# Optimization experiments

Measured on AMD Instinct MI355X. Metric: run time of the kernel, lower is better.

## Reference

```python
import jax, jax.numpy as jnp
import numpy as np

N_HEADS = 16
WINDOW_SIZE = 128


def setup_inputs() -> dict:
    key = jax.random.key(0)
    ks = jax.random.split(key, 5)
    B, T, D = 2, 2048, 1024
    x = jax.random.normal(ks[0], (B, T, D), dtype=jnp.float32)
    w_qkv = jax.random.normal(ks[1], (3 * D, D), dtype=jnp.float32) * (D ** -0.5)
    b_qkv = jax.random.normal(ks[2], (3 * D,), dtype=jnp.float32) * 0.01
    w_out = jax.random.normal(ks[3], (D, D), dtype=jnp.float32) * (D ** -0.5)
    b_out = jax.random.normal(ks[4], (D,), dtype=jnp.float32) * 0.01
    return {"x": x, "w_qkv": w_qkv, "b_qkv": b_qkv, "w_out": w_out, "b_out": b_out}


def reference(x, w_qkv, b_qkv, w_out, b_out):
    B, T, D = x.shape
    H = N_HEADS
    hd = D // H
    scale = hd ** -0.5

    # qkv projection: (B,T,3D) -> (3,B,H,T,hd)
    qkv = (x @ w_qkv.T + b_qkv).reshape(B, T, 3, H, hd)
    qkv = jnp.transpose(qkv, (2, 0, 3, 1, 4))
    q, k, v = qkv[0], qkv[1], qkv[2]

    pos = jnp.arange(T)
    # mask[i, j]: |j - i| <= w/2 and j >= i  (faithful to original, which
    # due to its index orientation allows query i to attend to keys j >= i)
    mask = (jnp.abs(pos[None, :] - pos[:, None]) <= WINDOW_SIZE // 2) & (
        pos[None, :] >= pos[:, None]
    )

    attn = jnp.einsum("bhqd,bhkd->bhqk", q, k) * scale  # (B,H,T,T)
    attn = jnp.where(mask[None, None], attn, -jnp.inf)
    attn = jax.nn.softmax(attn, axis=-1)
    attn = jnp.nan_to_num(attn, nan=0.0)

    out = jnp.einsum("bhqk,bhkd->bhqd", attn, v)  # (B,H,T,hd)
    out = jnp.transpose(out, (0, 2, 1, 3)).reshape(B, T, D)
    return out @ w_out.T + b_out
```

## Files before the change

kernel.cpp:

```cpp
#include <hip/hip_runtime.h>
#include <hip/hip_bf16.h>
#include <stdint.h>


typedef short bf16x8 __attribute__((ext_vector_type(8)));
typedef float f32x4 __attribute__((ext_vector_type(4)));

typedef const __attribute__((address_space(1))) void* gptr_t;
typedef __attribute__((address_space(3))) void* lptr_t;

__device__ __forceinline__ float bf2f(short u) {
    union { float f; uint32_t i; } x;
    x.i = ((uint32_t)(uint16_t)u) << 16;
    return x.f;
}
__device__ __forceinline__ short f2bf(float f) {
    __hip_bfloat16 h = __float2bfloat16(f);
    return *reinterpret_cast<short*>(&h);
}

__global__ __launch_bounds__(256)
void convert_all(const float* __restrict__ x, const float* __restrict__ wq,
                 const float* __restrict__ bq, const float* __restrict__ wo,
                 const float* __restrict__ bo,
                 short* __restrict__ xb, short* __restrict__ wqb, short* __restrict__ bqb,
                 short* __restrict__ wob, short* __restrict__ bob) {
    int i = blockIdx.x * 256 + threadIdx.x;
    const float* src; short* dst; int o;
    if      (i <  524288) { src = x;  dst = xb;  o = i; }
    else if (i <  917504) { src = wq; dst = wqb; o = i - 524288; }
    else if (i <  917888) { src = bq; dst = bqb; o = i - 917504; }
    else if (i < 1048960) { src = wo; dst = wob; o = i - 917888; }
    else if (i < 1049088) { src = bo; dst = bob; o = i - 1048960; }
    else return;
    const int e = o * 8;
    float4 a = *(const float4*)(src + e);
    float4 b = *(const float4*)(src + e + 4);
    short t[8];
    t[0] = f2bf(a.x); t[1] = f2bf(a.y); t[2] = f2bf(a.z); t[3] = f2bf(a.w);
    t[4] = f2bf(b.x); t[5] = f2bf(b.y); t[6] = f2bf(b.z); t[7] = f2bf(b.w);
    *(uint4*)(dst + e) = *(const uint4*)t;
}

__global__ __launch_bounds__(256)
void gemm_bt_128(const short* __restrict__ A, const short* __restrict__ Bt,
                 const short* __restrict__ bias, short* __restrict__ C,
                 int M, int N, int K) {
    __shared__ short As[128 * 32];
    __shared__ short Bs[128 * 32];

    const int tid  = threadIdx.x;
    const int lane = tid & 63;
    const int w    = tid >> 6;
    const int qd   = lane >> 4;
    const int l16  = lane & 15;
    const int wm   = w >> 1;
    const int wn   = w & 1;
    const int mBase = blockIdx.y * 128;
    const int nBase = blockIdx.x * 128;

    f32x4 acc[4][4] = {};

    const int nK = K >> 5;
    for (int kt = 0; kt < nK; ++kt) {
        const int kb = kt << 5;
#pragma unroll
        for (int i = 0; i < 2; ++i) {
            const int e   = i * 2048 + tid * 8;
            const int row = e >> 5;
            const int col = e & 31;
            const short* ga = A  + (size_t)(mBase + row) * K + kb + col;
            const short* gb = Bt + (size_t)(nBase + row) * K + kb + col;
            lptr_t la = (lptr_t)(As + i * 2048 + w * 512);
            lptr_t lb = (lptr_t)(Bs + i * 2048 + w * 512);
            __builtin_amdgcn_global_load_lds((gptr_t)ga, la, 16, 0, 0);
            __builtin_amdgcn_global_load_lds((gptr_t)gb, lb, 16, 0, 0);
        }
        __syncthreads();

        bf16x8 af[4], bfr[4];
#pragma unroll
        for (int mi = 0; mi < 4; ++mi)
            af[mi] = *(const bf16x8*)(As + (wm * 64 + mi * 16 + l16) * 32 + qd * 8);
#pragma unroll
        for (int ni = 0; ni < 4; ++ni)
            bfr[ni] = *(const bf16x8*)(Bs + (wn * 64 + ni * 16 + l16) * 32 + qd * 8);
#pragma unroll
        for (int mi = 0; mi < 4; ++mi)
#pragma unroll
            for (int ni = 0; ni < 4; ++ni)
                acc[mi][ni] = __builtin_amdgcn_mfma_f32_16x16x32_bf16(
                    bfr[ni], af[mi], acc[mi][ni], 0, 0, 0);
        __syncthreads();
    }

#pragma unroll
    for (int ni = 0; ni < 4; ++ni) {
        const int n0 = nBase + wn * 64 + ni * 16 + qd * 4;
        float bv[4];
#pragma unroll
        for (int r = 0; r < 4; ++r) bv[r] = bf2f(bias[n0 + r]);
#pragma unroll
        for (int mi = 0; mi < 4; ++mi) {
            const int m = mBase + wm * 64 + mi * 16 + l16;
            short t[4];
#pragma unroll
            for (int r = 0; r < 4; ++r) t[r] = f2bf(acc[mi][ni][r] + bv[r]);
            *(uint2*)&C[(size_t)m * N + n0] = *(const uint2*)t;
        }
    }
}

__global__ __launch_bounds__(256)
void gemm_bt_64(const short* __restrict__ A, const short* __restrict__ Bt,
                const short* __restrict__ bias, float* __restrict__ C,
                int M, int N, int K) {
    __shared__ short As[64 * 32];
    __shared__ short Bs[128 * 32];

    const int tid  = threadIdx.x;
    const int lane = tid & 63;
    const int w    = tid >> 6;
    const int qd   = lane >> 4;
    const int l16  = lane & 15;
    const int wm   = w >> 1;
    const int wn   = w & 1;
    const int mBase = blockIdx.y * 64;
    const int nBase = blockIdx.x * 128;

    f32x4 acc[2][4] = {};

    const int nK = K >> 5;
    for (int kt = 0; kt < nK; ++kt) {
        const int kb = kt << 5;
        {
            const int e   = tid * 8;
            const int row = e >> 5;
            const int col = e & 31;
            const short* ga = A + (size_t)(mBase + row) * K + kb + col;
            lptr_t la = (lptr_t)(As + w * 512);
            __builtin_amdgcn_global_load_lds((gptr_t)ga, la, 16, 0, 0);
        }
#pragma unroll
        for (int i = 0; i < 2; ++i) {
            const int e   = i * 2048 + tid * 8;
            const int row = e >> 5;
            const int col = e & 31;
            const short* gb = Bt + (size_t)(nBase + row) * K + kb + col;
            lptr_t lb = (lptr_t)(Bs + i * 2048 + w * 512);
            __builtin_amdgcn_global_load_lds((gptr_t)gb, lb, 16, 0, 0);
        }
        __syncthreads();

        bf16x8 af[2], bfr[4];
#pragma unroll
        for (int mi = 0; mi < 2; ++mi)
            af[mi] = *(const bf16x8*)(As + (wm * 32 + mi * 16 + l16) * 32 + qd * 8);
#pragma unroll
        for (int ni = 0; ni < 4; ++ni)
            bfr[ni] = *(const bf16x8*)(Bs + (wn * 64 + ni * 16 + l16) * 32 + qd * 8);
#pragma unroll
        for (int mi = 0; mi < 2; ++mi)
#pragma unroll
            for (int ni = 0; ni < 4; ++ni)
                acc[mi][ni] = __builtin_amdgcn_mfma_f32_16x16x32_bf16(
                    bfr[ni], af[mi], acc[mi][ni], 0, 0, 0);
        __syncthreads();
    }

#pragma unroll
    for (int ni = 0; ni < 4; ++ni) {
        const int n0 = nBase + wn * 64 + ni * 16 + qd * 4;
        float bv[4];
#pragma unroll
        for (int r = 0; r < 4; ++r) bv[r] = bf2f(bias[n0 + r]);
#pragma unroll
        for (int mi = 0; mi < 2; ++mi) {
            const int m = mBase + wm * 32 + mi * 16 + l16;
            f32x4 o;
#pragma unroll
            for (int r = 0; r < 4; ++r) o[r] = acc[mi][ni][r] + bv[r];
            *(f32x4*)&C[(size_t)m * N + n0] = o;
        }
    }
}

__global__ __launch_bounds__(256)
void attn_mfma(const short* __restrict__ qkv, short* __restrict__ attn_out, int B, int T) {
    __shared__ short k_s[128 * 72];
    __shared__ short v_s[144 * 66];
    __shared__ short p_s[64 * 104];

    const int tid  = threadIdx.x;
    const int lane = tid & 63;
    const int w    = tid >> 6;
    const int qd   = lane >> 4;
    const int l16  = lane & 15;
    const int qs   = blockIdx.x * 64;
    const int h    = blockIdx.y;
    const int b    = blockIdx.z;
    const size_t rs   = 3072;
    const size_t base = (size_t)b * T * rs;
    const int qoff = h * 64, koff = 1024 + h * 64, voff = 2048 + h * 64;

#pragma unroll
    for (int i = 0; i < 5; ++i) {
        const int c   = tid + i * 256;
        const int row = c >> 3;
        if (row >= 144) break;
        const int ch = (c & 7) * 8;
        int gr = qs + row; if (gr > T - 1) gr = T - 1;
        uint4 uv = *(const uint4*)(qkv + base + (size_t)gr * rs + voff + ch);
        if (row < 128) {
            uint4 uk = *(const uint4*)(qkv + base + (size_t)gr * rs + koff + ch);
            *(uint4*)&k_s[row * 72 + ch] = uk;
        }
        const uint32_t* vp = (const uint32_t*)&uv;
        uint32_t* vd = (uint32_t*)&v_s[row * 66 + ch];
        vd[0] = vp[0]; vd[1] = vp[1]; vd[2] = vp[2]; vd[3] = vp[3];
    }
    __syncthreads();

    bf16x8 aq0, aq1;
    {
        const short* g = qkv + base + (size_t)(qs + 16 * w + l16) * rs + qoff + qd * 8;
        aq0 = *(const bf16x8*)(g);
        aq1 = *(const bf16x8*)(g + 32);
    }

    f32x4 sacc[5] = {};
#pragma unroll
    for (int u = 0; u < 5; ++u) {
        const int krow = 16 * (w + u) + l16;
        bf16x8 bk0 = *(const bf16x8*)&k_s[krow * 72 + qd * 8];
        bf16x8 bk1 = *(const bf16x8*)&k_s[krow * 72 + 32 + qd * 8];
        sacc[u] = __builtin_amdgcn_mfma_f32_16x16x32_bf16(aq0, bk0, sacc[u], 0, 0, 0);
        sacc[u] = __builtin_amdgcn_mfma_f32_16x16x32_bf16(aq1, bk1, sacc[u], 0, 0, 0);
    }

    const float scale = 0.125f;
    float pw[5][4];
    float inv[4];
#pragma unroll
    for (int r = 0; r < 4; ++r) {
        const int m = 4 * qd + r;
        float mx = -3.4e38f;
#pragma unroll
        for (int u = 0; u < 5; ++u) {
            const int rel = 16 * u + l16 - m;
            const int j   = qs + 16 * (w + u) + l16;
            const bool ok = (rel >= 0) & (rel <= 64) & (j < T);
            const float v = ok ? sacc[u][r] * scale : -3.4e38f;
            pw[u][r] = v;
            mx = fmaxf(mx, v);
        }
#pragma unroll
        for (int msk = 1; msk <= 8; msk <<= 1) mx = fmaxf(mx, __shfl_xor(mx, msk));
        float sum = 0.f;
#pragma unroll
        for (int u = 0; u < 5; ++u) {
            float e = (pw[u][r] <= -3.0e38f) ? 0.f : __expf(pw[u][r] - mx);
            pw[u][r] = e;
            sum += e;
        }
#pragma unroll
        for (int msk = 1; msk <= 8; msk <<= 1) sum += __shfl_xor(sum, msk);
        inv[r] = 1.0f / sum;
    }

#pragma unroll
    for (int u = 0; u < 5; ++u)
#pragma unroll
        for (int r = 0; r < 4; ++r)
            p_s[(16 * w + 4 * qd + r) * 104 + 16 * u + l16] = f2bf(pw[u][r] * inv[r]);
#pragma unroll
    for (int r = 0; r < 4; ++r)
        p_s[(16 * w + 4 * qd + r) * 104 + 80 + l16] = 0;

    f32x4 oacc[4] = {};
#pragma unroll
    for (int ks = 0; ks < 3; ++ks) {
        bf16x8 ap = *(const bf16x8*)&p_s[(16 * w + l16) * 104 + ks * 32 + qd * 8];
#pragma unroll
        for (int dt = 0; dt < 4; ++dt) {
            short t[8];
#pragma unroll
            for (int j = 0; j < 8; ++j)
                t[j] = v_s[(16 * w + ks * 32 + qd * 8 + j) * 66 + 16 * dt + l16];
            bf16x8 bv = *(const bf16x8*)t;
            oacc[dt] = __builtin_amdgcn_mfma_f32_16x16x32_bf16(bv, ap, oacc[dt], 0, 0, 0);
        }
    }

    const size_t row = (size_t)(b * T + qs + 16 * w + l16);
#pragma unroll
    for (int dt = 0; dt < 4; ++dt) {
        short t[4];
#pragma unroll
        for (int r = 0; r < 4; ++r) t[r] = f2bf(oacc[dt][r]);
        *(uint2*)&attn_out[row * 1024 + h * 64 + dt * 16 + qd * 4] = *(const uint2*)t;
    }
}

extern "C" void kernel_launch(void* const* d_in, const int* in_sizes, int n_in,
                              void* d_out, int out_size, void* d_ws, size_t ws_size,
                              hipStream_t stream) {
    (void)in_sizes; (void)n_in; (void)out_size; (void)ws_size;
    const int B = 2, T = 2048, D = 1024;
    const int M = B * T;

    char* ws = (char*)d_ws;
    size_t off = 0;
    short* xb   = (short*)(ws + off); off += (size_t)M * D * 2;
    short* wqkb = (short*)(ws + off); off += (size_t)3 * D * D * 2;
    short* bqkb = (short*)(ws + off); off += (size_t)3 * D * 2;
    short* wob  = (short*)(ws + off); off += (size_t)D * D * 2;
    short* bob  = (short*)(ws + off); off += (size_t)D * 2;
    short* qkv  = (short*)(ws + off); off += (size_t)M * 3 * D * 2;
    short* attn = (short*)(ws + off); off += (size_t)M * D * 2;

    convert_all<<<dim3(4099), 256, 0, stream>>>(
        (const float*)d_in[0], (const float*)d_in[1], (const float*)d_in[2],
        (const float*)d_in[3], (const float*)d_in[4], xb, wqkb, bqkb, wob, bob);

    gemm_bt_128<<<dim3(3 * D / 128, M / 128), 256, 0, stream>>>(
        xb, wqkb, bqkb, qkv, M, 3 * D, D);
    attn_mfma<<<dim3(T / 64, 16, B), 256, 0, stream>>>(qkv, attn, B, T);
    gemm_bt_64<<<dim3(D / 128, M / 64), 256, 0, stream>>>(
        attn, wob, bob, (float*)d_out, M, D, D);
}
```

Measured before the change: 164.5 us.

## Use fp32 biases directly, remap GEMM block order, enlarge output GEMM tile

Bias vectors are no longer converted to bf16 and are read as fp32 inside the GEMMs. The QKV GEMM now uses a 1D grid with a grouped tile order intended to improve L2 reuse. The output GEMM moves from 64x128 to 128x128 tiles, halving its block count. The MFMA operand order is swapped, so epilogue stores become scalar per-element writes (2-byte bf16 stores, 4-byte fp32 stores) instead of vector writes, which may cost store bandwidth.

```diff
diff --git a/kernel.cpp b/kernel.cpp
--- a/kernel.cpp
+++ b/kernel.cpp
@@ -21,18 +21,13 @@
 
 __global__ __launch_bounds__(256)
 void convert_all(const float* __restrict__ x, const float* __restrict__ wq,
-                 const float* __restrict__ bq, const float* __restrict__ wo,
-                 const float* __restrict__ bo,
-                 short* __restrict__ xb, short* __restrict__ wqb, short* __restrict__ bqb,
-                 short* __restrict__ wob, short* __restrict__ bob) {
+                 const float* __restrict__ wo,
+                 short* __restrict__ xb, short* __restrict__ wqb, short* __restrict__ wob) {
     int i = blockIdx.x * 256 + threadIdx.x;
     const float* src; short* dst; int o;
     if      (i <  524288) { src = x;  dst = xb;  o = i; }
     else if (i <  917504) { src = wq; dst = wqb; o = i - 524288; }
-    else if (i <  917888) { src = bq; dst = bqb; o = i - 917504; }
-    else if (i < 1048960) { src = wo; dst = wob; o = i - 917888; }
-    else if (i < 1049088) { src = bo; dst = bob; o = i - 1048960; }
-    else return;
+    else                  { src = wo; dst = wob; o = i - 917504; }
     const int e = o * 8;
     float4 a = *(const float4*)(src + e);
     float4 b = *(const float4*)(src + e + 4);
@@ -43,11 +38,17 @@
 }
 
 __global__ __launch_bounds__(256)
-void gemm_bt_128(const short* __restrict__ A, const short* __restrict__ Bt,
-                 const short* __restrict__ bias, short* __restrict__ C,
-                 int M, int N, int K) {
+void gemm1_qkv(const short* __restrict__ A, const short* __restrict__ Bt,
+               const float* __restrict__ bias, short* __restrict__ C,
+               int M, int N, int K) {
     __shared__ short As[128 * 32];
     __shared__ short Bs[128 * 32];
+
+    const int bid = blockIdx.x;
+    const int g   = bid & 7;
+    const int r   = bid >> 3;
+    const int xt  = g + 8 * (r % 3);
+    const int yt  = r / 3;
 
     const int tid  = threadIdx.x;
     const int lane = tid & 63;
@@ -56,8 +57,8 @@
     const int l16  = lane & 15;
     const int wm   = w >> 1;
     const int wn   = w & 1;
-    const int mBase = blockIdx.y * 128;
-    const int nBase = blockIdx.x * 128;
+    const int mBase = yt * 128;
+    const int nBase = xt * 128;
 
     f32x4 acc[4][4] = {};
 
@@ -90,33 +91,34 @@
 #pragma unroll
             for (int ni = 0; ni < 4; ++ni)
                 acc[mi][ni] = __builtin_amdgcn_mfma_f32_16x16x32_bf16(
-                    bfr[ni], af[mi], acc[mi][ni], 0, 0, 0);
+                    af[mi], bfr[ni], acc[mi][ni], 0, 0, 0);
         __syncthreads();
     }
 
 #pragma unroll
     for (int ni = 0; ni < 4; ++ni) {
-        const int n0 = nBase + wn * 64 + ni * 16 + qd * 4;
-        float bv[4];
-#pragma unroll
-        for (int r = 0; r < 4; ++r) bv[r] = bf2f(bias[n0 + r]);
-#pragma unroll
-        for (int mi = 0; mi < 4; ++mi) {
-            const int m = mBase + wm * 64 + mi * 16 + l16;
-            short t[4];
-#pragma unroll
-            for (int r = 0; r < 4; ++r) t[r] = f2bf(acc[mi][ni][r] + bv[r]);
-            *(uint2*)&C[(size_t)m * N + n0] = *(const uint2*)t;
-        }
+        const int n = nBase + wn * 64 + ni * 16 + l16;
+        const float bv = bias[n];
+#pragma unroll
+        for (int mi = 0; mi < 4; ++mi)
+#pragma unroll
+            for (int rr = 0; rr < 4; ++rr) {
+                const int m = mBase + wm * 64 + mi * 16 + qd * 4 + rr;
+                C[(size_t)m * N + n] = f2bf(acc[mi][ni][rr] + bv);
+            }
     }
 }
 
 __global__ __launch_bounds__(256)
-void gemm_bt_64(const short* __restrict__ A, const short* __restrict__ Bt,
-                const short* __restrict__ bias, float* __restrict__ C,
-                int M, int N, int K) {
-    __shared__ short As[64 * 32];
+void gemm2_out(const short* __restrict__ A, const short* __restrict__ Bt,
+               const float* __restrict__ bias, float* __restrict__ C,
+               int M, int N, int K) {
+    __shared__ short As[128 * 32];
     __shared__ short Bs[128 * 32];
+
+    const int bid = blockIdx.x;
+    const int xt  = bid & 7;
+    const int yt  = bid >> 3;
 
     const int tid  = threadIdx.x;
     const int lane = tid & 63;
@@ -125,63 +127,55 @@
     const int l16  = lane & 15;
     const int wm   = w >> 1;
     const int wn   = w & 1;
-    const int mBase = blockIdx.y * 64;
-    const int nBase = blockIdx.x * 128;
-
-    f32x4 acc[2][4] = {};
+    const int mBase = yt * 128;
+    const int nBase = xt * 128;
+
+    f32x4 acc[4][4] = {};
 
     const int nK = K >> 5;
     for (int kt = 0; kt < nK; ++kt) {
         const int kb = kt << 5;
-        {
-            const int e   = tid * 8;
-            const int row = e >> 5;
-            const int col = e & 31;
-            const short* ga = A + (size_t)(mBase + row) * K + kb + col;
-            lptr_t la = (lptr_t)(As + w * 512);
-            __builtin_amdgcn_global_load_lds((gptr_t)ga, la, 16, 0, 0);
-        }
 #pragma unroll
         for (int i = 0; i < 2; ++i) {
             const int e   = i * 2048 + tid * 8;
             const int row = e >> 5;
             const int col = e & 31;
+            const short* ga = A  + (size_t)(mBase + row) * K + kb + col;
             const short* gb = Bt + (size_t)(nBase + row) * K + kb + col;
+            lptr_t la = (lptr_t)(As + i * 2048 + w * 512);
             lptr_t lb = (lptr_t)(Bs + i * 2048 + w * 512);
+            __builtin_amdgcn_global_load_lds((gptr_t)ga, la, 16, 0, 0);
             __builtin_amdgcn_global_load_lds((gptr_t)gb, lb, 16, 0, 0);
         }
         __syncthreads();
 
-        bf16x8 af[2], bfr[4];
-#pragma unroll
-        for (int mi = 0; mi < 2; ++mi)
-            af[mi] = *(const bf16x8*)(As + (wm * 32 + mi * 16 + l16) * 32 + qd * 8);
+        bf16x8 af[4], bfr[4];
+#pragma unroll
+        for (int mi = 0; mi < 4; ++mi)
+            af[mi] = *(const bf16x8*)(As + (wm * 64 + mi * 16 + l16) * 32 + qd * 8);
 #pragma unroll
         for (int ni = 0; ni < 4; ++ni)
             bfr[ni] = *(const bf16x8*)(Bs + (wn * 64 + ni * 16 + l16) * 32 + qd * 8);
 #pragma unroll
-        for (int mi = 0; mi < 2; ++mi)
+        for (int mi = 0; mi < 4; ++mi)
 #pragma unroll
             for (int ni = 0; ni < 4; ++ni)
                 acc[mi][ni] = __builtin_amdgcn_mfma_f32_16x16x32_bf16(
-                    bfr[ni], af[mi], acc[mi][ni], 0, 0, 0);
+                    af[mi], bfr[ni], acc[mi][ni], 0, 0, 0);
         __syncthreads();
     }
 
 #pragma unroll
     for (int ni = 0; ni < 4; ++ni) {
-        const int n0 = nBase + wn * 64 + ni * 16 + qd * 4;
-        float bv[4];
-#pragma unroll
-        for (int r = 0; r < 4; ++r) bv[r] = bf2f(bias[n0 + r]);
-#pragma unroll
-        for (int mi = 0; mi < 2; ++mi) {
-            const int m = mBase + wm * 32 + mi * 16 + l16;
-            f32x4 o;
-#pragma unroll
-            for (int r = 0; r < 4; ++r) o[r] = acc[mi][ni][r] + bv[r];
-            *(f32x4*)&C[(size_t)m * N + n0] = o;
-        }
+        const int n = nBase + wn * 64 + ni * 16 + l16;
+        const float bv = bias[n];
+#pragma unroll
+        for (int mi = 0; mi < 4; ++mi)
+#pragma unroll
+            for (int rr = 0; rr < 4; ++rr) {
+                const int m = mBase + wm * 64 + mi * 16 + qd * 4 + rr;
+                C[(size_t)m * N + n] = acc[mi][ni][rr] + bv;
+            }
     }
 }
 
@@ -313,19 +307,17 @@
     size_t off = 0;
     short* xb   = (short*)(ws + off); off += (size_t)M * D * 2;
     short* wqkb = (short*)(ws + off); off += (size_t)3 * D * D * 2;
-    short* bqkb = (short*)(ws + off); off += (size_t)3 * D * 2;
     short* wob  = (short*)(ws + off); off += (size_t)D * D * 2;
-    short* bob  = (short*)(ws + off); off += (size_t)D * 2;
     short* qkv  = (short*)(ws + off); off += (size_t)M * 3 * D * 2;
     short* attn = (short*)(ws + off); off += (size_t)M * D * 2;
 
-    convert_all<<<dim3(4099), 256, 0, stream>>>(
-        (const float*)d_in[0], (const float*)d_in[1], (const float*)d_in[2],
-        (const float*)d_in[3], (const float*)d_in[4], xb, wqkb, bqkb, wob, bob);
-
-    gemm_bt_128<<<dim3(3 * D / 128, M / 128), 256, 0, stream>>>(
-        xb, wqkb, bqkb, qkv, M, 3 * D, D);
+    convert_all<<<dim3(4096), 256, 0, stream>>>(
+        (const float*)d_in[0], (const float*)d_in[1], (const float*)d_in[3],
+        xb, wqkb, wob);
+
+    gemm1_qkv<<<dim3(768), 256, 0, stream>>>(
+        xb, wqkb, (const float*)d_in[2], qkv, M, 3 * D, D);
     attn_mfma<<<dim3(T / 64, 16, B), 256, 0, stream>>>(qkv, attn, B, T);
-    gemm_bt_64<<<dim3(D / 128, M / 64), 256, 0, stream>>>(
-        attn, wob, bob, (float*)d_out, M, D, D);
-}
+    gemm2_out<<<dim3(256), 256, 0, stream>>>(
+        attn, wob, (const float*)d_in[4], (float*)d_out, M, D, D);
+}
```

After: 161.6 us. No clear change (-1.8%).
